# Kernel tuning notes

Hardware: AMD Instinct MI355X
Metric: run time of the kernel (lower is better)

The kernel has to match this reference:

```python
import jax, jax.numpy as jnp
import numpy as np

NUM_CLASSES = 80
NUM_TOP_QUERIES = 300


def setup_inputs() -> dict:
    key = jax.random.key(0)
    k1, k2, k3 = jax.random.split(key, 3)
    B, Q, C = 256, 1000, NUM_CLASSES
    logits = jax.random.normal(k1, (B, Q, C), dtype=jnp.float32)
    # cxcywh boxes in [0,1)
    boxes = jax.random.uniform(k2, (B, Q, 4), dtype=jnp.float32)
    # image (w, h) sizes in [320, 960)
    orig_target_sizes = 320.0 + 640.0 * jax.random.uniform(k3, (B, 2), dtype=jnp.float32)
    return {"logits": logits, "boxes": boxes, "orig_target_sizes": orig_target_sizes}


def _box_cxcywh_to_xyxy(b):
    cx, cy, w, h = b[..., 0], b[..., 1], b[..., 2], b[..., 3]
    half_w, half_h = 0.5 * w, 0.5 * h
    return jnp.stack([cx - half_w, cy - half_h, cx + half_w, cy + half_h], axis=-1)


def reference(logits, boxes, orig_target_sizes):
    B, Q, C = logits.shape
    # box decode: cxcywh -> xyxy, scale to image size (w,h,w,h)
    bbox_pred = _box_cxcywh_to_xyxy(boxes)
    scale = jnp.tile(orig_target_sizes, (1, 2))[:, None, :]  # [B,1,4]
    bbox_pred = bbox_pred * scale
    # focal-loss path: sigmoid scores, flattened topk over Q*C
    scores = jax.nn.sigmoid(logits).reshape(B, Q * C)
    scores, index = jax.lax.top_k(scores, NUM_TOP_QUERIES)  # [B,K]
    labels = index % C
    qidx = index // C
    boxes_sel = jnp.take_along_axis(bbox_pred, qidx[..., None], axis=1)  # [B,K,4]
    return labels, boxes_sel, scores
```

## Files before the change

kernel.cpp:

```cpp
#include <hip/hip_runtime.h>
#include <cstdint>

#define NB 256
#define NQ 1000
#define NC 80
#define QC 80000
#define TOPK 300
#define PREFILTER 2.2f
#define CHUNKS 8
#define CCAP 256
#define LCAP 320
#define T1 256
#define T2 256
#define GCAP (CHUNKS * CCAP)
#define SORT2 512

#define WS_CAND_OFF 8192
#define WS_NEEDED (WS_CAND_OFF + (size_t)NB * CHUNKS * CCAP * 8)

__device__ __forceinline__ uint32_t fkey(uint32_t u) {
  return (u & 0x80000000u) ? ~u : (u | 0x80000000u);
}

__global__ __launch_bounds__(T1) void prefilter_kernel(
    const float* __restrict__ logits,
    uint32_t* __restrict__ counters,
    uint64_t* __restrict__ cand) {
  __shared__ uint64_t buf[LCAP];
  __shared__ int cnt;
  const int blk = blockIdx.x;
  const int b = blk >> 3;
  const int chunk = blk & 7;
  const int tid = threadIdx.x;
  if (tid == 0) cnt = 0;
  __syncthreads();

  const int n4 = QC / 4 / CHUNKS;
  const float4* lg4 = (const float4*)(logits + (size_t)b * QC) + chunk * n4;
  for (int i = tid; i < n4; i += T1) {
    float4 v = lg4[i];
    const int gbase = (chunk * n4 + i) * 4;
    float comp[4] = {v.x, v.y, v.z, v.w};
#pragma unroll
    for (int c = 0; c < 4; ++c) {
      float x = comp[c];
      if (x > PREFILTER) {
        uint32_t idx = (uint32_t)(gbase + c);
        int pos = atomicAdd(&cnt, 1);
        if (pos < LCAP)
          buf[pos] = ((uint64_t)fkey(__float_as_uint(x)) << 32) | (uint32_t)(~idx);
      }
    }
  }
  __syncthreads();
  int c = cnt;
  if (c > CCAP) c = CCAP;
  if (tid == 0) counters[blk] = (uint32_t)c;
  uint64_t* dst = cand + (size_t)blk * CCAP;
  for (int i = tid; i < c; i += T1) dst[i] = buf[i];
}

__global__ __launch_bounds__(T2) void select_kernel(
    const uint32_t* __restrict__ counters,
    const uint64_t* __restrict__ cand,
    const float* __restrict__ boxes,
    const float* __restrict__ sizes,
    float* __restrict__ out) {
  __shared__ uint64_t cs[GCAP];
  __shared__ uint64_t sortBuf[SORT2];
  __shared__ uint32_t hist[256];
  __shared__ uint32_t scanb[256];
  __shared__ int sNsort;
  __shared__ int sKRem;
  __shared__ uint32_t sDigit;

  const int b = blockIdx.x;
  const int tid = threadIdx.x;
  if (tid == 0) sNsort = 0;

  uint32_t cj[CHUNKS];
  int off[CHUNKS];
  int count = 0;
#pragma unroll
  for (int j = 0; j < CHUNKS; ++j) {
    cj[j] = counters[b * CHUNKS + j];
    off[j] = count;
    count += (int)cj[j];
  }
#pragma unroll
  for (int j = 0; j < CHUNKS; ++j) {
    const uint64_t* src = cand + (size_t)(b * CHUNKS + j) * CCAP;
    for (int i = tid; i < (int)cj[j]; i += T2) cs[off[j] + i] = src[i];
  }
  __syncthreads();

  uint32_t prefix = 0, mask = 0;
  int kRem = TOPK;
  for (int r = 3; r >= 0; --r) {
    const int sh = r * 8;
    hist[tid] = 0;
    __syncthreads();
    for (int i = tid; i < count; i += T2) {
      uint32_t key = (uint32_t)(cs[i] >> 32);
      if ((key & mask) == prefix) atomicAdd(&hist[(key >> sh) & 255], 1u);
    }
    __syncthreads();
    scanb[tid] = hist[tid];
    __syncthreads();
    for (int s = 1; s < 256; s <<= 1) {
      uint32_t add = (tid + s < 256) ? scanb[tid + s] : 0u;
      __syncthreads();
      scanb[tid] += add;
      __syncthreads();
    }
    {
      bool p  = (scanb[tid] >= (uint32_t)kRem);
      bool pn = (tid < 255) && (scanb[tid + 1] >= (uint32_t)kRem);
      if (p && !pn) {
        sDigit = (uint32_t)tid;
        sKRem  = kRem - (int)(scanb[tid] - hist[tid]);
      }
    }
    __syncthreads();
    prefix |= sDigit << sh;
    mask   |= 0xFFu << sh;
    kRem    = sKRem;
    __syncthreads();
  }
  const uint32_t T = prefix;

  for (int i = tid; i < count; i += T2) {
    uint64_t item = cs[i];
    if ((uint32_t)(item >> 32) >= T) {
      int pos = atomicAdd(&sNsort, 1);
      if (pos < SORT2) sortBuf[pos] = item;
    }
  }
  __syncthreads();
  int nsort = sNsort;
  if (nsort > SORT2) nsort = SORT2;
  for (int i = tid; i < SORT2; i += T2)
    if (i >= nsort) sortBuf[i] = 0;
  __syncthreads();

  for (int k = 2; k <= SORT2; k <<= 1) {
    for (int j = k >> 1; j > 0; j >>= 1) {
      const int i1 = ((tid & ~(j - 1)) << 1) | (tid & (j - 1));
      const int i2 = i1 | j;
      uint64_t a = sortBuf[i1];
      uint64_t c = sortBuf[i2];
      const bool dirDesc = ((i1 & k) == 0);
      if (dirDesc ? (a < c) : (a > c)) { sortBuf[i1] = c; sortBuf[i2] = a; }
      __syncthreads();
    }
  }

  for (int t = tid; t < TOPK; t += T2) {
    const uint64_t item = sortBuf[t];
    const uint32_t key = (uint32_t)(item >> 32);
    const uint32_t idx = ~((uint32_t)item);
    const int q  = (int)(idx / NC);
    const int cl = (int)(idx - (uint32_t)q * NC);
    const uint32_t u = (key & 0x80000000u) ? (key ^ 0x80000000u) : ~key;
    const float x = __uint_as_float(u);
    const float score = 1.0f / (1.0f + expf(-x));

    const float4 bx = ((const float4*)boxes)[b * NQ + q];
    const float W = sizes[2 * b];
    const float H = sizes[2 * b + 1];
    const float hw = 0.5f * bx.z;
    const float hh = 0.5f * bx.w;

    out[b * TOPK + t] = (float)cl;
    float* ob = out + (size_t)NB * TOPK + ((size_t)b * TOPK + t) * 4;
    ob[0] = (bx.x - hw) * W;
    ob[1] = (bx.y - hh) * H;
    ob[2] = (bx.x + hw) * W;
    ob[3] = (bx.y + hh) * H;
    out[(size_t)NB * TOPK * 5 + b * TOPK + t] = score;
  }
}

#define CAND_CAP 6144
#define SORT_CAP 1024
#define NTHREADS 1024

__global__ __launch_bounds__(NTHREADS) void rtdetr_post_fallback(
    const float* __restrict__ logits,
    const float* __restrict__ boxes,
    const float* __restrict__ sizes,
    float* __restrict__ out) {
  __shared__ uint64_t candL[CAND_CAP];
  __shared__ uint64_t sortBuf[SORT_CAP];
  __shared__ uint32_t hist[256];
  __shared__ uint32_t scanb[256];
  __shared__ int sCount;
  __shared__ int sNsort;
  __shared__ int sKRem;
  __shared__ uint32_t sDigit;

  const int b   = blockIdx.x;
  const int tid = threadIdx.x;

  if (tid == 0) { sCount = 0; sNsort = 0; }
  __syncthreads();

  const float4* lg4 = (const float4*)(logits + (size_t)b * QC);
  for (int i = tid; i < QC / 4; i += NTHREADS) {
    float4 v = lg4[i];
    float comp[4] = {v.x, v.y, v.z, v.w};
#pragma unroll
    for (int c = 0; c < 4; ++c) {
      float x = comp[c];
      if (x > 2.0f) {
        uint32_t k = fkey(__float_as_uint(x));
        uint32_t idx = (uint32_t)(i * 4 + c);
        int pos = atomicAdd(&sCount, 1);
        if (pos < CAND_CAP) candL[pos] = ((uint64_t)k << 32) | (uint32_t)(~idx);
      }
    }
  }
  __syncthreads();
  int count = sCount;
  if (count > CAND_CAP) count = CAND_CAP;

  uint32_t prefix = 0, mask = 0;
  int kRem = TOPK;
  for (int r = 3; r >= 0; --r) {
    const int sh = r * 8;
    if (tid < 256) hist[tid] = 0;
    __syncthreads();
    for (int i = tid; i < count; i += NTHREADS) {
      uint32_t key = (uint32_t)(candL[i] >> 32);
      if ((key & mask) == prefix) atomicAdd(&hist[(key >> sh) & 255], 1u);
    }
    __syncthreads();
    if (tid < 256) scanb[tid] = hist[tid];
    __syncthreads();
    for (int s = 1; s < 256; s <<= 1) {
      uint32_t add = 0;
      if (tid < 256 && tid + s < 256) add = scanb[tid + s];
      __syncthreads();
      if (tid < 256) scanb[tid] += add;
      __syncthreads();
    }
    if (tid < 256) {
      bool p  = (scanb[tid] >= (uint32_t)kRem);
      bool pn = (tid < 255) && (scanb[tid + 1] >= (uint32_t)kRem);
      if (p && !pn) {
        sDigit = (uint32_t)tid;
        sKRem  = kRem - (int)(scanb[tid] - hist[tid]);
      }
    }
    __syncthreads();
    prefix |= sDigit << sh;
    mask   |= 0xFFu << sh;
    kRem    = sKRem;
    __syncthreads();
  }
  const uint32_t T = prefix;

  for (int i = tid; i < count; i += NTHREADS) {
    uint64_t item = candL[i];
    if ((uint32_t)(item >> 32) >= T) {
      int pos = atomicAdd(&sNsort, 1);
      if (pos < SORT_CAP) sortBuf[pos] = item;
    }
  }
  __syncthreads();
  int nsort = sNsort;
  if (nsort > SORT_CAP) nsort = SORT_CAP;
  for (int i = tid; i < SORT_CAP; i += NTHREADS)
    if (i >= nsort) sortBuf[i] = 0;
  __syncthreads();

  for (int k = 2; k <= SORT_CAP; k <<= 1) {
    for (int j = k >> 1; j > 0; j >>= 1) {
      const int i = tid;
      const int l = i ^ j;
      if (l > i) {
        uint64_t a = sortBuf[i];
        uint64_t c = sortBuf[l];
        const bool dirDesc = ((i & k) == 0);
        if (dirDesc ? (a < c) : (a > c)) { sortBuf[i] = c; sortBuf[l] = a; }
      }
      __syncthreads();
    }
  }

  if (tid < TOPK) {
    const uint64_t item = sortBuf[tid];
    const uint32_t key = (uint32_t)(item >> 32);
    const uint32_t idx = ~((uint32_t)item);
    const int q  = (int)(idx / NC);
    const int cl = (int)(idx - (uint32_t)q * NC);
    const uint32_t u = (key & 0x80000000u) ? (key ^ 0x80000000u) : ~key;
    const float x = __uint_as_float(u);
    const float score = 1.0f / (1.0f + expf(-x));

    const float4 bx = ((const float4*)boxes)[b * NQ + q];
    const float W = sizes[2 * b];
    const float H = sizes[2 * b + 1];
    const float hw = 0.5f * bx.z;
    const float hh = 0.5f * bx.w;

    out[b * TOPK + tid] = (float)cl;
    float* ob = out + (size_t)NB * TOPK + ((size_t)b * TOPK + tid) * 4;
    ob[0] = (bx.x - hw) * W;
    ob[1] = (bx.y - hh) * H;
    ob[2] = (bx.x + hw) * W;
    ob[3] = (bx.y + hh) * H;
    out[(size_t)NB * TOPK * 5 + b * TOPK + tid] = score;
  }
}

extern "C" void kernel_launch(void* const* d_in, const int* in_sizes, int n_in,
                              void* d_out, int out_size, void* d_ws, size_t ws_size,
                              hipStream_t stream) {
  const float* logits = (const float*)d_in[0];
  const float* boxes  = (const float*)d_in[1];
  const float* sizes  = (const float*)d_in[2];
  float* out = (float*)d_out;
  (void)in_sizes; (void)n_in; (void)out_size;

  if (ws_size >= WS_NEEDED) {
    uint32_t* counters = (uint32_t*)d_ws;
    uint64_t* cand = (uint64_t*)((char*)d_ws + WS_CAND_OFF);
    prefilter_kernel<<<dim3(NB * CHUNKS), dim3(T1), 0, stream>>>(logits, counters, cand);
    select_kernel<<<dim3(NB), dim3(T2), 0, stream>>>(counters, cand, boxes, sizes, out);
  } else {
    rtdetr_post_fallback<<<dim3(NB), dim3(NTHREADS), 0, stream>>>(logits, boxes, sizes, out);
  }
}
```

Measured before the change: 137.5 us.

## Fuse prefilter and select kernels using last-block-done atomic counter

Merges the prefilter and top-k select stages into one kernel. Each chunk block writes its candidates to global memory and bumps a per-batch atomic counter, and the last block to finish for a batch performs the radix select, bitonic sort and box gather. The change also replaces the shared-memory suffix scan with wavefront shuffles and skips the per-element checks when no lane of a float4 passes the threshold. It adds a memset launch, threadfence ordering, and a larger per-block shared-memory footprint on the filter blocks, which could lower occupancy during the memory-bound scan.

```diff
diff --git a/kernel.cpp b/kernel.cpp
--- a/kernel.cpp
+++ b/kernel.cpp
@@ -6,119 +6,126 @@
 #define NC 80
 #define QC 80000
 #define TOPK 300
-#define PREFILTER 2.2f
+#define PF 2.2f
 #define CHUNKS 8
 #define CCAP 256
-#define LCAP 320
 #define T1 256
-#define T2 256
 #define GCAP (CHUNKS * CCAP)
 #define SORT2 512
 
-#define WS_CAND_OFF 8192
-#define WS_NEEDED (WS_CAND_OFF + (size_t)NB * CHUNKS * CCAP * 8)
+#define WS_CNT_OFF 1024
+#define WS_CAND_OFF 16384
+#define WS_NEEDED (WS_CAND_OFF + (size_t)NB * GCAP * 8)
 
 __device__ __forceinline__ uint32_t fkey(uint32_t u) {
   return (u & 0x80000000u) ? ~u : (u | 0x80000000u);
 }
 
-__global__ __launch_bounds__(T1) void prefilter_kernel(
+__global__ __launch_bounds__(T1) void fused_kernel(
     const float* __restrict__ logits,
-    uint32_t* __restrict__ counters,
-    uint64_t* __restrict__ cand) {
-  __shared__ uint64_t buf[LCAP];
-  __shared__ int cnt;
+    const float* __restrict__ boxes,
+    const float* __restrict__ sizes,
+    uint32_t* __restrict__ done,
+    uint32_t* __restrict__ cnts,
+    uint64_t* __restrict__ cand,
+    float* __restrict__ out) {
+  __shared__ uint64_t cs[GCAP];
+  __shared__ uint64_t sortBuf[SORT2];
+  __shared__ uint32_t hist[256];
+  __shared__ uint32_t sufx[256];
+  __shared__ uint32_t wtot[4];
+  __shared__ int sCnt;
+  __shared__ int sNsort;
+  __shared__ int sKRem;
+  __shared__ uint32_t sDigit;
+  __shared__ int sLast;
+
   const int blk = blockIdx.x;
   const int b = blk >> 3;
   const int chunk = blk & 7;
   const int tid = threadIdx.x;
-  if (tid == 0) cnt = 0;
+  if (tid == 0) { sCnt = 0; sNsort = 0; }
   __syncthreads();
 
   const int n4 = QC / 4 / CHUNKS;
   const float4* lg4 = (const float4*)(logits + (size_t)b * QC) + chunk * n4;
   for (int i = tid; i < n4; i += T1) {
     float4 v = lg4[i];
-    const int gbase = (chunk * n4 + i) * 4;
-    float comp[4] = {v.x, v.y, v.z, v.w};
-#pragma unroll
-    for (int c = 0; c < 4; ++c) {
-      float x = comp[c];
-      if (x > PREFILTER) {
-        uint32_t idx = (uint32_t)(gbase + c);
-        int pos = atomicAdd(&cnt, 1);
-        if (pos < LCAP)
-          buf[pos] = ((uint64_t)fkey(__float_as_uint(x)) << 32) | (uint32_t)(~idx);
-      }
-    }
-  }
-  __syncthreads();
-  int c = cnt;
-  if (c > CCAP) c = CCAP;
-  if (tid == 0) counters[blk] = (uint32_t)c;
-  uint64_t* dst = cand + (size_t)blk * CCAP;
-  for (int i = tid; i < c; i += T1) dst[i] = buf[i];
-}
-
-__global__ __launch_bounds__(T2) void select_kernel(
-    const uint32_t* __restrict__ counters,
-    const uint64_t* __restrict__ cand,
-    const float* __restrict__ boxes,
-    const float* __restrict__ sizes,
-    float* __restrict__ out) {
-  __shared__ uint64_t cs[GCAP];
-  __shared__ uint64_t sortBuf[SORT2];
-  __shared__ uint32_t hist[256];
-  __shared__ uint32_t scanb[256];
-  __shared__ int sNsort;
-  __shared__ int sKRem;
-  __shared__ uint32_t sDigit;
-
-  const int b = blockIdx.x;
-  const int tid = threadIdx.x;
-  if (tid == 0) sNsort = 0;
+    if (v.x > PF || v.y > PF || v.z > PF || v.w > PF) {
+      const int gbase = (chunk * n4 + i) * 4;
+      float comp[4] = {v.x, v.y, v.z, v.w};
+#pragma unroll
+      for (int c = 0; c < 4; ++c) {
+        if (comp[c] > PF) {
+          int pos = atomicAdd(&sCnt, 1);
+          if (pos < CCAP)
+            cs[pos] = ((uint64_t)fkey(__float_as_uint(comp[c])) << 32) |
+                      (uint32_t)(~(uint32_t)(gbase + c));
+        }
+      }
+    }
+  }
+  __syncthreads();
+  int myc = sCnt;
+  if (myc > CCAP) myc = CCAP;
+  uint64_t* dstc = cand + (size_t)blk * CCAP;
+  for (int i = tid; i < myc; i += T1) dstc[i] = cs[i];
+  if (tid == 0) cnts[blk] = (uint32_t)myc;
+
+  __threadfence();
+  if (tid == 0) sLast = (atomicAdd(&done[b], 1u) == CHUNKS - 1) ? 1 : 0;
+  __syncthreads();
+  if (!sLast) return;
+  __threadfence();
 
   uint32_t cj[CHUNKS];
   int off[CHUNKS];
   int count = 0;
 #pragma unroll
   for (int j = 0; j < CHUNKS; ++j) {
-    cj[j] = counters[b * CHUNKS + j];
+    cj[j] = cnts[b * CHUNKS + j];
     off[j] = count;
     count += (int)cj[j];
   }
 #pragma unroll
   for (int j = 0; j < CHUNKS; ++j) {
     const uint64_t* src = cand + (size_t)(b * CHUNKS + j) * CCAP;
-    for (int i = tid; i < (int)cj[j]; i += T2) cs[off[j] + i] = src[i];
-  }
-  __syncthreads();
-
+    for (int i = tid; i < (int)cj[j]; i += T1) cs[off[j] + i] = src[i];
+  }
+  __syncthreads();
+
+  const int lane = tid & 63;
+  const int w = tid >> 6;
   uint32_t prefix = 0, mask = 0;
   int kRem = TOPK;
   for (int r = 3; r >= 0; --r) {
     const int sh = r * 8;
     hist[tid] = 0;
     __syncthreads();
-    for (int i = tid; i < count; i += T2) {
+    for (int i = tid; i < count; i += T1) {
       uint32_t key = (uint32_t)(cs[i] >> 32);
       if ((key & mask) == prefix) atomicAdd(&hist[(key >> sh) & 255], 1u);
     }
     __syncthreads();
-    scanb[tid] = hist[tid];
-    __syncthreads();
-    for (int s = 1; s < 256; s <<= 1) {
-      uint32_t add = (tid + s < 256) ? scanb[tid + s] : 0u;
-      __syncthreads();
-      scanb[tid] += add;
-      __syncthreads();
-    }
+    uint32_t v = hist[tid];
+#pragma unroll
+    for (int s = 1; s < 64; s <<= 1) {
+      uint32_t o = __shfl_down(v, s, 64);
+      if (lane + s < 64) v += o;
+    }
+    if (lane == 0) wtot[w] = v;
+    __syncthreads();
+#pragma unroll
+    for (int j = 0; j < 4; ++j)
+      if (j > w) v += wtot[j];
+    sufx[tid] = v;
+    __syncthreads();
     {
-      bool p  = (scanb[tid] >= (uint32_t)kRem);
-      bool pn = (tid < 255) && (scanb[tid + 1] >= (uint32_t)kRem);
+      bool p  = (v >= (uint32_t)kRem);
+      bool pn = (tid < 255) && (sufx[tid + 1] >= (uint32_t)kRem);
       if (p && !pn) {
         sDigit = (uint32_t)tid;
-        sKRem  = kRem - (int)(scanb[tid] - hist[tid]);
+        sKRem  = kRem - (int)(v - hist[tid]);
       }
     }
     __syncthreads();
@@ -129,7 +136,7 @@
   }
   const uint32_t T = prefix;
 
-  for (int i = tid; i < count; i += T2) {
+  for (int i = tid; i < count; i += T1) {
     uint64_t item = cs[i];
     if ((uint32_t)(item >> 32) >= T) {
       int pos = atomicAdd(&sNsort, 1);
@@ -139,7 +146,7 @@
   __syncthreads();
   int nsort = sNsort;
   if (nsort > SORT2) nsort = SORT2;
-  for (int i = tid; i < SORT2; i += T2)
+  for (int i = tid; i < SORT2; i += T1)
     if (i >= nsort) sortBuf[i] = 0;
   __syncthreads();
 
@@ -155,7 +162,7 @@
     }
   }
 
-  for (int t = tid; t < TOPK; t += T2) {
+  for (int t = tid; t < TOPK; t += T1) {
     const uint64_t item = sortBuf[t];
     const uint32_t key = (uint32_t)(item >> 32);
     const uint32_t idx = ~((uint32_t)item);
@@ -324,10 +331,12 @@
   (void)in_sizes; (void)n_in; (void)out_size;
 
   if (ws_size >= WS_NEEDED) {
-    uint32_t* counters = (uint32_t*)d_ws;
+    uint32_t* done = (uint32_t*)d_ws;
+    uint32_t* cnts = (uint32_t*)((char*)d_ws + WS_CNT_OFF);
     uint64_t* cand = (uint64_t*)((char*)d_ws + WS_CAND_OFF);
-    prefilter_kernel<<<dim3(NB * CHUNKS), dim3(T1), 0, stream>>>(logits, counters, cand);
-    select_kernel<<<dim3(NB), dim3(T2), 0, stream>>>(counters, cand, boxes, sizes, out);
+    hipMemsetAsync(d_ws, 0, NB * sizeof(uint32_t), stream);
+    fused_kernel<<<dim3(NB * CHUNKS), dim3(T1), 0, stream>>>(
+        logits, boxes, sizes, done, cnts, cand, out);
   } else {
     rtdetr_post_fallback<<<dim3(NB), dim3(NTHREADS), 0, stream>>>(logits, boxes, sizes, out);
   }
```

Result: slower. 456.7 us (+232.2%).

## Use wave shuffles for radix scan and bitonic sort, exit radix select early

Applied to the files above, without the earlier changes.

The select kernel now runs 512 threads, one per sort element. The bitonic sort keeps each element in a register and uses cross-lane xor shuffles for strides below 64, so it touches LDS and barriers only for the larger strides. The histogram suffix scan becomes a wave shuffle scan plus per-wave totals, and the radix select stops once the candidate set above the threshold fits in the sort buffer. The prefilter skips the per-component loop when no lane of the float4 passes the threshold. These changes target barrier-heavy serial phases in a small per-batch kernel, and they rely on SORT2 equalling T2.

```diff
diff --git a/kernel.cpp b/kernel.cpp
--- a/kernel.cpp
+++ b/kernel.cpp
@@ -6,12 +6,12 @@
 #define NC 80
 #define QC 80000
 #define TOPK 300
-#define PREFILTER 2.2f
+#define PF 2.2f
 #define CHUNKS 8
 #define CCAP 256
 #define LCAP 320
 #define T1 256
-#define T2 256
+#define T2 512
 #define GCAP (CHUNKS * CCAP)
 #define SORT2 512
 
@@ -39,16 +39,17 @@
   const float4* lg4 = (const float4*)(logits + (size_t)b * QC) + chunk * n4;
   for (int i = tid; i < n4; i += T1) {
     float4 v = lg4[i];
-    const int gbase = (chunk * n4 + i) * 4;
-    float comp[4] = {v.x, v.y, v.z, v.w};
-#pragma unroll
-    for (int c = 0; c < 4; ++c) {
-      float x = comp[c];
-      if (x > PREFILTER) {
-        uint32_t idx = (uint32_t)(gbase + c);
-        int pos = atomicAdd(&cnt, 1);
-        if (pos < LCAP)
-          buf[pos] = ((uint64_t)fkey(__float_as_uint(x)) << 32) | (uint32_t)(~idx);
+    if (v.x > PF || v.y > PF || v.z > PF || v.w > PF) {
+      const int gbase = (chunk * n4 + i) * 4;
+      float comp[4] = {v.x, v.y, v.z, v.w};
+#pragma unroll
+      for (int c = 0; c < 4; ++c) {
+        if (comp[c] > PF) {
+          int pos = atomicAdd(&cnt, 1);
+          if (pos < LCAP)
+            buf[pos] = ((uint64_t)fkey(__float_as_uint(comp[c])) << 32) |
+                       (uint32_t)(~(uint32_t)(gbase + c));
+        }
       }
     }
   }
@@ -69,10 +70,12 @@
   __shared__ uint64_t cs[GCAP];
   __shared__ uint64_t sortBuf[SORT2];
   __shared__ uint32_t hist[256];
-  __shared__ uint32_t scanb[256];
+  __shared__ uint32_t sufx[256];
+  __shared__ uint32_t wtot[4];
   __shared__ int sNsort;
   __shared__ int sKRem;
   __shared__ uint32_t sDigit;
+  __shared__ uint32_t sSuf;
 
   const int b = blockIdx.x;
   const int tid = threadIdx.x;
@@ -95,39 +98,53 @@
   __syncthreads();
 
   uint32_t prefix = 0, mask = 0;
+  uint32_t T = 0;
   int kRem = TOPK;
   for (int r = 3; r >= 0; --r) {
     const int sh = r * 8;
-    hist[tid] = 0;
+    if (tid < 256) hist[tid] = 0;
     __syncthreads();
     for (int i = tid; i < count; i += T2) {
       uint32_t key = (uint32_t)(cs[i] >> 32);
       if ((key & mask) == prefix) atomicAdd(&hist[(key >> sh) & 255], 1u);
     }
     __syncthreads();
-    scanb[tid] = hist[tid];
-    __syncthreads();
-    for (int s = 1; s < 256; s <<= 1) {
-      uint32_t add = (tid + s < 256) ? scanb[tid + s] : 0u;
-      __syncthreads();
-      scanb[tid] += add;
-      __syncthreads();
-    }
-    {
-      bool p  = (scanb[tid] >= (uint32_t)kRem);
-      bool pn = (tid < 255) && (scanb[tid + 1] >= (uint32_t)kRem);
+    uint32_t v = 0;
+    if (tid < 256) {
+      const int lane = tid & 63;
+      v = hist[tid];
+#pragma unroll
+      for (int s = 1; s < 64; s <<= 1) {
+        uint32_t o = __shfl_down(v, s, 64);
+        if (lane + s < 64) v += o;
+      }
+      if (lane == 0) wtot[tid >> 6] = v;
+    }
+    __syncthreads();
+    if (tid < 256) {
+      const int w = tid >> 6;
+#pragma unroll
+      for (int j = 0; j < 4; ++j)
+        if (j > w) v += wtot[j];
+      sufx[tid] = v;
+    }
+    __syncthreads();
+    if (tid < 256) {
+      bool p  = (sufx[tid] >= (uint32_t)kRem);
+      bool pn = (tid < 255) && (sufx[tid + 1] >= (uint32_t)kRem);
       if (p && !pn) {
         sDigit = (uint32_t)tid;
-        sKRem  = kRem - (int)(scanb[tid] - hist[tid]);
+        sKRem  = kRem - (int)(sufx[tid] - hist[tid]);
+        sSuf   = sufx[tid];
       }
     }
     __syncthreads();
     prefix |= sDigit << sh;
     mask   |= 0xFFu << sh;
     kRem    = sKRem;
-    __syncthreads();
-  }
-  const uint32_t T = prefix;
+    T       = prefix;
+    if (sSuf <= (uint32_t)SORT2) break;
+  }
 
   for (int i = tid; i < count; i += T2) {
     uint64_t item = cs[i];
@@ -139,24 +156,31 @@
   __syncthreads();
   int nsort = sNsort;
   if (nsort > SORT2) nsort = SORT2;
-  for (int i = tid; i < SORT2; i += T2)
-    if (i >= nsort) sortBuf[i] = 0;
-  __syncthreads();
-
+  if (tid >= nsort) sortBuf[tid] = 0;
+  __syncthreads();
+
+  uint64_t v = sortBuf[tid];
   for (int k = 2; k <= SORT2; k <<= 1) {
+    const bool up = ((tid & k) == 0);
     for (int j = k >> 1; j > 0; j >>= 1) {
-      const int i1 = ((tid & ~(j - 1)) << 1) | (tid & (j - 1));
-      const int i2 = i1 | j;
-      uint64_t a = sortBuf[i1];
-      uint64_t c = sortBuf[i2];
-      const bool dirDesc = ((i1 & k) == 0);
-      if (dirDesc ? (a < c) : (a > c)) { sortBuf[i1] = c; sortBuf[i2] = a; }
-      __syncthreads();
-    }
-  }
-
-  for (int t = tid; t < TOPK; t += T2) {
-    const uint64_t item = sortBuf[t];
+      uint64_t o;
+      if (j < 64) {
+        o = __shfl_xor((unsigned long long)v, j, 64);
+      } else {
+        sortBuf[tid] = v;
+        __syncthreads();
+        o = sortBuf[tid ^ j];
+        __syncthreads();
+      }
+      const bool keepMax = (((tid & j) == 0) == up);
+      v = keepMax ? (v > o ? v : o) : (v < o ? v : o);
+    }
+  }
+  sortBuf[tid] = v;
+  __syncthreads();
+
+  if (tid < TOPK) {
+    const uint64_t item = sortBuf[tid];
     const uint32_t key = (uint32_t)(item >> 32);
     const uint32_t idx = ~((uint32_t)item);
     const int q  = (int)(idx / NC);
@@ -171,13 +195,13 @@
     const float hw = 0.5f * bx.z;
     const float hh = 0.5f * bx.w;
 
-    out[b * TOPK + t] = (float)cl;
-    float* ob = out + (size_t)NB * TOPK + ((size_t)b * TOPK + t) * 4;
+    out[b * TOPK + tid] = (float)cl;
+    float* ob = out + (size_t)NB * TOPK + ((size_t)b * TOPK + tid) * 4;
     ob[0] = (bx.x - hw) * W;
     ob[1] = (bx.y - hh) * H;
     ob[2] = (bx.x + hw) * W;
     ob[3] = (bx.y + hh) * H;
-    out[(size_t)NB * TOPK * 5 + b * TOPK + t] = score;
+    out[(size_t)NB * TOPK * 5 + b * TOPK + tid] = score;
   }
 }
 
```

Measured after the change: 132.3 us. 1.04x faster.
